# Performance work log

Measured on AMD Instinct MI355X. Metric: run time of the kernel, lower is better.

Reference implementation:

```python
import jax, jax.numpy as jnp
import numpy as np

M_MARGIN = 0.25
GAMMA = 64.0
EPS = 1e-5


def _circle_loss_one_way(enc, dec):
    # enc, dec: [N, D]. Faithful to the torch rotate-concat construction:
    # cos_sim[j, k] = cosine(enc[j], dec[(j + k) % N]); column 0 is the positive.
    N = enc.shape[0]
    dot = enc @ dec.T                                   # [N, N]
    en = jnp.sqrt(jnp.sum(enc * enc, axis=1, keepdims=True))   # [N, 1]
    dn = jnp.sqrt(jnp.sum(dec * dec, axis=1, keepdims=True))   # [N, 1]
    S = dot / (en * dn.T + EPS)                         # [N, N] cosine sims
    r = jnp.arange(N)
    idx = (r[:, None] + r[None, :]) % N                 # [N, N] rolled column index
    cos_sim = jnp.take_along_axis(S, idx, axis=1)       # [N, N]
    sp = cos_sim[:, 0:1]                                # [N, 1] positives (diag of S)
    sn = cos_sim[:, 1:]                                 # [N, N-1] negatives
    ap = jnp.maximum(-jax.lax.stop_gradient(sp) + 1.0 + M_MARGIN, 0.0)
    an = jnp.maximum(jax.lax.stop_gradient(sn) + M_MARGIN, 0.0)
    delta_p = 1.0 - M_MARGIN
    delta_n = M_MARGIN
    logit_p = -ap * (sp - delta_p) * GAMMA              # [N, 1]
    logit_n = an * (sn - delta_n) * GAMMA               # [N, N-1]
    lse_n = jax.nn.logsumexp(logit_n, axis=0)           # [N-1]
    lse_p = jax.nn.logsumexp(logit_p, axis=0)           # [1] (cols of repeated sp are identical)
    return jax.nn.softplus(lse_n + lse_p)               # [N-1]


def reference(encoder_output, decoder_output):
    loss_a = _circle_loss_one_way(encoder_output, decoder_output)
    loss_b = _circle_loss_one_way(decoder_output, encoder_output)
    return jnp.mean((loss_a + loss_b) / 2.0)


def setup_inputs() -> dict:
    key = jax.random.key(0)
    k1, k2 = jax.random.split(key)
    N, D = 8192, 128
    return {
        "encoder_output": jax.random.normal(k1, (N, D), dtype=jnp.float32),
        "decoder_output": jax.random.normal(k2, (N, D), dtype=jnp.float32),
    }
```

## Files before the change

### kernel.cpp

```cpp
#include <hip/hip_runtime.h>
#include <hip/hip_bf16.h>

#define NN 8192

using f32x4 = __attribute__((ext_vector_type(4))) float;

#if __has_builtin(__builtin_amdgcn_exp2f)
#define EXP2(x) __builtin_amdgcn_exp2f(x)
#else
#define EXP2(x) __expf((x) * 0.69314718056f)
#endif

__device__ __forceinline__ void gl_lds16(const void* g, void* l) {
  __builtin_amdgcn_global_load_lds(
      (const __attribute__((address_space(1))) unsigned int*)(unsigned long long)g,
      (__attribute__((address_space(3))) unsigned int*)(unsigned int)(unsigned long long)l,
      16, 0, 0);
}

#define BAR_VMCNT4() asm volatile("s_waitcnt vmcnt(4)\n\ts_barrier" ::: "memory")

#if __has_builtin(__builtin_amdgcn_cvt_pk_fp8_f32)
__device__ __forceinline__ unsigned pk4_fp8(float x0, float x1, float x2, float x3) {
  unsigned w = (unsigned)__builtin_amdgcn_cvt_pk_fp8_f32(x0, x1, 0, false);
  w = (unsigned)__builtin_amdgcn_cvt_pk_fp8_f32(x2, x3, (int)w, true);
  return w;
}
#else
__device__ __forceinline__ unsigned f8_1(float f) {
  unsigned u = __float_as_uint(f);
  unsigned s = (u >> 24) & 0x80u;
  float a = fabsf(f);
  if (a < 0.015625f) {
    unsigned m = (unsigned)rintf(a * 512.0f);
    return s | (m > 7u ? 8u : m);
  }
  if (a > 448.0f) return s | 0x7Eu;
  unsigned au = u & 0x7FFFFFFFu;
  unsigned e = (au >> 23) - 127u + 7u;
  unsigned m23 = au & 0x7FFFFFu;
  unsigned m = m23 >> 20;
  unsigned rem = m23 & 0xFFFFFu;
  if (rem > 0x80000u || (rem == 0x80000u && (m & 1u))) {
    if (++m == 8u) { m = 0u; ++e; }
  }
  return s | (e << 3) | m;
}
__device__ __forceinline__ unsigned pk4_fp8(float x0, float x1, float x2, float x3) {
  return f8_1(x0) | (f8_1(x1) << 8) | (f8_1(x2) << 16) | (f8_1(x3) << 24);
}
#endif

__global__ __launch_bounds__(256) void k_prep(const float* __restrict__ enc,
                                              const float* __restrict__ dec,
                                              uint2* __restrict__ A8,
                                              uint2* __restrict__ B8,
                                              float* __restrict__ logit_p,
                                              float* __restrict__ bandsum,
                                              unsigned* __restrict__ counter) {
  const int t = threadIdx.x;
  const int l16 = t & 15;
  const int row = blockIdx.x * 16 + (t >> 4);
  const int tid = blockIdx.x * 256 + t;
  if (tid < 64 * 256) bandsum[tid] = 0.0f;
  if (tid == 64 * 256) *counter = 0u;

  const float4* e4 = reinterpret_cast<const float4*>(enc) + (size_t)row * 32 + l16 * 2;
  const float4* d4 = reinterpret_cast<const float4*>(dec) + (size_t)row * 32 + l16 * 2;
  float4 e0 = e4[0], e1 = e4[1];
  float4 d0 = d4[0], d1 = d4[1];

  float se = e0.x*e0.x + e0.y*e0.y + e0.z*e0.z + e0.w*e0.w
           + e1.x*e1.x + e1.y*e1.y + e1.z*e1.z + e1.w*e1.w;
  float sd = d0.x*d0.x + d0.y*d0.y + d0.z*d0.z + d0.w*d0.w
           + d1.x*d1.x + d1.y*d1.y + d1.z*d1.z + d1.w*d1.w;
  float sp = e0.x*d0.x + e0.y*d0.y + e0.z*d0.z + e0.w*d0.w
           + e1.x*d1.x + e1.y*d1.y + e1.z*d1.z + e1.w*d1.w;
#pragma unroll
  for (int off = 1; off < 16; off <<= 1) {
    se += __shfl_xor(se, off);
    sd += __shfl_xor(sd, off);
    sp += __shfl_xor(sp, off);
  }
  float ie = rsqrtf(se), id = rsqrtf(sd);

  uint2 ua, ub;
  ua.x = pk4_fp8(e0.x * ie, e0.y * ie, e0.z * ie, e0.w * ie);
  ua.y = pk4_fp8(e1.x * ie, e1.y * ie, e1.z * ie, e1.w * ie);
  ub.x = pk4_fp8(d0.x * id, d0.y * id, d0.z * id, d0.w * id);
  ub.y = pk4_fp8(d1.x * id, d1.y * id, d1.z * id, d1.w * id);
  A8[(size_t)row * 16 + l16] = ua;
  B8[(size_t)row * 16 + l16] = ub;

  if (l16 == 0) {
    float en = se * ie, dn = sd * id;
    float s  = sp / (en * dn + 1e-5f);
    logit_p[row] = -fmaxf(1.25f - s, 0.0f) * (s - 0.75f) * 64.0f;
  }
}

__global__ __launch_bounds__(256, 3) void k_main(const unsigned char* __restrict__ A,
                                                 const unsigned char* __restrict__ B,
                                                 float* __restrict__ bandsum,
                                                 const float* __restrict__ logit_p,
                                                 unsigned* __restrict__ counter,
                                                 float* __restrict__ out) {
  __shared__ __align__(16) unsigned char As[3 * 8192];
  __shared__ __align__(16) unsigned char Bs[3 * 8192];
  __shared__ float part[4][256];
  __shared__ unsigned lastFlag;

  const int t  = threadIdx.x;
  const int T  = blockIdx.x;
  const int sp = blockIdx.y;

#pragma unroll
  for (int q = 0; q < 4; ++q) part[q][t] = 0.0f;

  const int lane = t & 63;
  const int w = t >> 6, wrow = w >> 1, wcol = w & 1;
  const int l15 = lane & 15, quad = lane >> 4;
  const int x3 = l15 & 3;
  const int qh = quad >> 1, ql8 = (quad & 1) * 8;

  const int lg    = (t >> 2) * 128 + (((t & 3) ^ ((t >> 2) & 3)) * 16);
  const int lloff = t * 16;

  const char* Ab = (const char*)A;
  const char* Bb = (const char*)B;

  float dreg[28];
#pragma unroll
  for (int i = 0; i < 28; ++i) dreg[i] = 0.0f;

  const int arow = (wrow * 64 + l15) * 64;
  const int brow = (wcol * 64 + l15) * 64;

  const int s16 = sp * 16;
  const int by0 = s16 / 3;
  const int by1 = (s16 + 16) / 3;
  const int H   = (by1 - by0) * 2;

  {
    const int bx = (by0 + T) & 63;
    const char* Ag = Ab + (size_t)by0 * 16384 + lg;
    const char* Bg = Bb + (size_t)bx * 16384 + lg;
#pragma unroll
    for (int j = 0; j < 2; ++j) {
      gl_lds16(Ag + j * 8192, (char*)As + j * 4096 + lloff);
      gl_lds16(Bg + j * 8192, (char*)Bs + j * 4096 + lloff);
    }
#pragma unroll
    for (int j = 0; j < 2; ++j) {
      gl_lds16(Ag + 64 + j * 8192, (char*)As + 8192 + j * 4096 + lloff);
      gl_lds16(Bg + 64 + j * 8192, (char*)Bs + 8192 + j * 4096 + lloff);
    }
  }
  BAR_VMCNT4();

  f32x4 acc[4][4];
  int cur = 0;

  for (int h = 0; h < H; ++h) {
    if (h + 2 < H) {
      const int hn = h + 2;
      const int by = by0 + (hn >> 1);
      const int bx = (by + T) & 63;
      int r2 = cur + 2; if (r2 >= 3) r2 -= 3;
      const char* Ag = Ab + (size_t)by * 16384 + (hn & 1) * 64 + lg;
      const char* Bg = Bb + (size_t)bx * 16384 + (hn & 1) * 64 + lg;
      char* Ad = (char*)As + r2 * 8192 + lloff;
      char* Bd = (char*)Bs + r2 * 8192 + lloff;
#pragma unroll
      for (int j = 0; j < 2; ++j) {
        gl_lds16(Ag + j * 8192, Ad + j * 4096);
        gl_lds16(Bg + j * 8192, Bd + j * 4096);
      }
    }

    if ((h & 1) == 0) {
      const f32x4 zv = {0.f, 0.f, 0.f, 0.f};
#pragma unroll
      for (int r = 0; r < 4; ++r)
#pragma unroll
        for (int c = 0; c < 4; ++c) acc[r][c] = zv;
    }

    const char* Abuf = (const char*)As + cur * 8192;
    const char* Bbuf = (const char*)Bs + cur * 8192;

#pragma unroll
    for (int ks = 0; ks < 2; ++ks) {
      long a[4], b[4];
      const int off = (((ks * 2 + qh) ^ x3) * 16) + ql8;
#pragma unroll
      for (int r = 0; r < 4; ++r)
        a[r] = *reinterpret_cast<const long*>(Abuf + arow + r * 1024 + off);
#pragma unroll
      for (int c = 0; c < 4; ++c)
        b[c] = *reinterpret_cast<const long*>(Bbuf + brow + c * 1024 + off);
#pragma unroll
      for (int r = 0; r < 4; ++r)
#pragma unroll
        for (int c = 0; c < 4; ++c)
          acc[r][c] = __builtin_amdgcn_mfma_f32_16x16x32_fp8_fp8(a[r], b[c], acc[r][c], 0, 0, 0);
    }

    if (h & 1) {
#pragma unroll
      for (int dlt = -3; dlt <= 3; ++dlt) {
#pragma unroll
        for (int g = 0; g < 4; ++g) {
          float s = 0.0f;
#pragma unroll
          for (int r = 0; r < 4; ++r) {
            int c = r + dlt;
            if (c < 0 || c > 3) continue;
            float sn = acc[r][c][g];
            float an = fmaxf(sn + 0.25f, 0.0f);
            float u  = fmaf(sn, 92.332483f, -23.083121f);
            s += EXP2(an * u);
          }
          dreg[(dlt + 3) * 4 + g] += s;
        }
      }
    }

    BAR_VMCNT4();
    if (++cur == 3) cur = 0;
  }

  const int  Qoff = (wcol - wrow) * 64 + 127;
  const int  v    = l15 - quad * 4;
  const bool leader = (quad == 0) || (l15 <= 3);
  const bool ok1 = (l15 <= 11) && (quad <= 2);
  const bool ok2 = (l15 <= 7)  && (quad <= 1);

#pragma unroll
  for (int dlt = -3; dlt <= 3; ++dlt) {
#pragma unroll
    for (int g = 0; g < 4; ++g) {
      float s = dreg[(dlt + 3) * 4 + g];
      float t1 = __shfl_down(s, 20); s += ok1 ? t1 : 0.0f;
      float t2 = __shfl_down(s, 40); s += ok2 ? t2 : 0.0f;
      int ld = Qoff + dlt * 16 - g + v;
      if (leader) unsafeAtomicAdd(&part[w][ld], s);
    }
  }
  __syncthreads();

  if (t < 255) {
    float vv = part[0][t] + part[1][t] + part[2][t] + part[3][t];
    unsafeAtomicAdd(&bandsum[T * 256 + t], vv);
  }

  __syncthreads();
  if (t == 0) lastFlag = (atomicAdd(counter, 1u) == 767u) ? 1u : 0u;
  __syncthreads();
  if (!lastFlag) return;

  __threadfence();
  float* sm = part[0];

  float lp[32];
#pragma unroll
  for (int k = 0; k < 32; ++k) lp[k] = logit_p[t + 256 * k];

  float m = lp[0];
#pragma unroll
  for (int k = 1; k < 32; ++k) m = fmaxf(m, lp[k]);
#pragma unroll
  for (int off = 32; off; off >>= 1) m = fmaxf(m, __shfl_down(m, off));
  if (lane == 0) sm[w] = m;
  __syncthreads();
  m = fmaxf(fmaxf(sm[0], sm[1]), fmaxf(sm[2], sm[3]));
  __syncthreads();

  float s = 0.0f;
#pragma unroll
  for (int k = 0; k < 32; ++k) s += __expf(lp[k] - m);
#pragma unroll
  for (int off = 32; off; off >>= 1) s += __shfl_down(s, off);
  if (lane == 0) sm[w] = s;
  __syncthreads();
  s = sm[0] + sm[1] + sm[2] + sm[3];
  float lse_p = m + __logf(s);
  __syncthreads();

  const int o  = t & 127;
  const int hi = t >> 7;
  float bs1[32], bs2[32];
#pragma unroll
  for (int k = 0; k < 32; ++k) {
    int Ta = hi + 2 * k;
    bs1[k] = bandsum[Ta * 256 + o + 127];
    bs2[k] = o ? bandsum[((Ta + 1) & 63) * 256 + o - 1] : 0.0f;
  }
  float tacc = 0.0f;
#pragma unroll
  for (int k = 0; k < 32; ++k) {
    if (t == 0 && k == 0) continue;
    float se = bs1[k] + bs2[k];
    float x = __logf(se) + lse_p;
    tacc += fmaxf(x, 0.0f) + __logf(1.0f + __expf(-fabsf(x)));
  }
#pragma unroll
  for (int off = 32; off; off >>= 1) tacc += __shfl_down(tacc, off);
  if (lane == 0) sm[w] = tacc;
  __syncthreads();
  if (t == 0) out[0] = (sm[0] + sm[1] + sm[2] + sm[3]) * (1.0f / 8191.0f);
}

extern "C" void kernel_launch(void* const* d_in, const int* in_sizes, int n_in,
                              void* d_out, int out_size, void* d_ws, size_t ws_size,
                              hipStream_t stream) {
  const float* enc = (const float*)d_in[0];
  const float* dec = (const float*)d_in[1];
  float* ws = (float*)d_ws;

  float*    logit_p = ws;
  float*    bandsum = ws + 8192;
  unsigned* counter = (unsigned*)(ws + 8192 + 16384);
  uint2*    A8      = (uint2*)(ws + 8192 + 16384 + 256);
  uint2*    B8      = (uint2*)((char*)A8 + 1048576);
  float*    out     = (float*)d_out;

  k_prep<<<NN / 16, 256, 0, stream>>>(enc, dec, A8, B8, logit_p, bandsum, counter);
  dim3 grid(64, 12);
  k_main<<<grid, 256, 0, stream>>>((const unsigned char*)A8, (const unsigned char*)B8,
                                   bandsum, logit_p, counter, out);
}
```

Measured before the change: 105.4 us.

## Load MFMA operands directly from global memory instead of LDS triple buffer

Removes the triple-buffered LDS staging, which used global_load_lds copies with barriers. Each wave now reads its fp8 A/B fragments straight from global memory (L1/L2) and processes a whole 128-deep K tile per iteration. This drops LDS traffic, barriers and LDS allocation, which may allow higher occupancy. In exchange every element is loaded redundantly by several waves from cache, and there is no explicit prefetch to overlap load latency with MFMA.

```diff
diff --git a/kernel.cpp b/kernel.cpp
--- a/kernel.cpp
+++ b/kernel.cpp
@@ -10,15 +10,6 @@
 #else
 #define EXP2(x) __expf((x) * 0.69314718056f)
 #endif
-
-__device__ __forceinline__ void gl_lds16(const void* g, void* l) {
-  __builtin_amdgcn_global_load_lds(
-      (const __attribute__((address_space(1))) unsigned int*)(unsigned long long)g,
-      (__attribute__((address_space(3))) unsigned int*)(unsigned int)(unsigned long long)l,
-      16, 0, 0);
-}
-
-#define BAR_VMCNT4() asm volatile("s_waitcnt vmcnt(4)\n\ts_barrier" ::: "memory")
 
 #if __has_builtin(__builtin_amdgcn_cvt_pk_fp8_f32)
 __device__ __forceinline__ unsigned pk4_fp8(float x0, float x1, float x2, float x3) {
@@ -105,8 +96,6 @@
                                                  const float* __restrict__ logit_p,
                                                  unsigned* __restrict__ counter,
                                                  float* __restrict__ out) {
-  __shared__ __align__(16) unsigned char As[3 * 8192];
-  __shared__ __align__(16) unsigned char Bs[3 * 8192];
   __shared__ float part[4][256];
   __shared__ unsigned lastFlag;
 
@@ -120,65 +109,30 @@
   const int lane = t & 63;
   const int w = t >> 6, wrow = w >> 1, wcol = w & 1;
   const int l15 = lane & 15, quad = lane >> 4;
-  const int x3 = l15 & 3;
-  const int qh = quad >> 1, ql8 = (quad & 1) * 8;
-
-  const int lg    = (t >> 2) * 128 + (((t & 3) ^ ((t >> 2) & 3)) * 16);
-  const int lloff = t * 16;
-
+
+  float dreg[28];
+#pragma unroll
+  for (int i = 0; i < 28; ++i) dreg[i] = 0.0f;
+
+  __syncthreads();
+
+  const int aoff = (wrow * 64 + l15) * 128 + quad * 8;
+  const int boff = (wcol * 64 + l15) * 128 + quad * 8;
   const char* Ab = (const char*)A;
   const char* Bb = (const char*)B;
-
-  float dreg[28];
-#pragma unroll
-  for (int i = 0; i < 28; ++i) dreg[i] = 0.0f;
-
-  const int arow = (wrow * 64 + l15) * 64;
-  const int brow = (wcol * 64 + l15) * 64;
 
   const int s16 = sp * 16;
   const int by0 = s16 / 3;
   const int by1 = (s16 + 16) / 3;
-  const int H   = (by1 - by0) * 2;
-
-  {
-    const int bx = (by0 + T) & 63;
-    const char* Ag = Ab + (size_t)by0 * 16384 + lg;
-    const char* Bg = Bb + (size_t)bx * 16384 + lg;
-#pragma unroll
-    for (int j = 0; j < 2; ++j) {
-      gl_lds16(Ag + j * 8192, (char*)As + j * 4096 + lloff);
-      gl_lds16(Bg + j * 8192, (char*)Bs + j * 4096 + lloff);
-    }
-#pragma unroll
-    for (int j = 0; j < 2; ++j) {
-      gl_lds16(Ag + 64 + j * 8192, (char*)As + 8192 + j * 4096 + lloff);
-      gl_lds16(Bg + 64 + j * 8192, (char*)Bs + 8192 + j * 4096 + lloff);
-    }
-  }
-  BAR_VMCNT4();
 
   f32x4 acc[4][4];
-  int cur = 0;
-
-  for (int h = 0; h < H; ++h) {
-    if (h + 2 < H) {
-      const int hn = h + 2;
-      const int by = by0 + (hn >> 1);
-      const int bx = (by + T) & 63;
-      int r2 = cur + 2; if (r2 >= 3) r2 -= 3;
-      const char* Ag = Ab + (size_t)by * 16384 + (hn & 1) * 64 + lg;
-      const char* Bg = Bb + (size_t)bx * 16384 + (hn & 1) * 64 + lg;
-      char* Ad = (char*)As + r2 * 8192 + lloff;
-      char* Bd = (char*)Bs + r2 * 8192 + lloff;
-#pragma unroll
-      for (int j = 0; j < 2; ++j) {
-        gl_lds16(Ag + j * 8192, Ad + j * 4096);
-        gl_lds16(Bg + j * 8192, Bd + j * 4096);
-      }
-    }
-
-    if ((h & 1) == 0) {
+
+  for (int by = by0; by < by1; ++by) {
+    const int bx = (by + T) & 63;
+    const char* Ag = Ab + (size_t)by * 16384 + aoff;
+    const char* Bg = Bb + (size_t)bx * 16384 + boff;
+
+    {
       const f32x4 zv = {0.f, 0.f, 0.f, 0.f};
 #pragma unroll
       for (int r = 0; r < 4; ++r)
@@ -186,19 +140,16 @@
         for (int c = 0; c < 4; ++c) acc[r][c] = zv;
     }
 
-    const char* Abuf = (const char*)As + cur * 8192;
-    const char* Bbuf = (const char*)Bs + cur * 8192;
-
-#pragma unroll
-    for (int ks = 0; ks < 2; ++ks) {
+#pragma unroll
+    for (int ks = 0; ks < 4; ++ks) {
       long a[4], b[4];
-      const int off = (((ks * 2 + qh) ^ x3) * 16) + ql8;
+      const int o = ks * 32;
 #pragma unroll
       for (int r = 0; r < 4; ++r)
-        a[r] = *reinterpret_cast<const long*>(Abuf + arow + r * 1024 + off);
+        a[r] = *reinterpret_cast<const long*>(Ag + r * 2048 + o);
 #pragma unroll
       for (int c = 0; c < 4; ++c)
-        b[c] = *reinterpret_cast<const long*>(Bbuf + brow + c * 1024 + off);
+        b[c] = *reinterpret_cast<const long*>(Bg + c * 2048 + o);
 #pragma unroll
       for (int r = 0; r < 4; ++r)
 #pragma unroll
@@ -206,28 +157,23 @@
           acc[r][c] = __builtin_amdgcn_mfma_f32_16x16x32_fp8_fp8(a[r], b[c], acc[r][c], 0, 0, 0);
     }
 
-    if (h & 1) {
-#pragma unroll
-      for (int dlt = -3; dlt <= 3; ++dlt) {
-#pragma unroll
-        for (int g = 0; g < 4; ++g) {
-          float s = 0.0f;
-#pragma unroll
-          for (int r = 0; r < 4; ++r) {
-            int c = r + dlt;
-            if (c < 0 || c > 3) continue;
-            float sn = acc[r][c][g];
-            float an = fmaxf(sn + 0.25f, 0.0f);
-            float u  = fmaf(sn, 92.332483f, -23.083121f);
-            s += EXP2(an * u);
-          }
-          dreg[(dlt + 3) * 4 + g] += s;
+#pragma unroll
+    for (int dlt = -3; dlt <= 3; ++dlt) {
+#pragma unroll
+      for (int g = 0; g < 4; ++g) {
+        float s = 0.0f;
+#pragma unroll
+        for (int r = 0; r < 4; ++r) {
+          int c = r + dlt;
+          if (c < 0 || c > 3) continue;
+          float sn = acc[r][c][g];
+          float an = fmaxf(sn + 0.25f, 0.0f);
+          float u  = fmaf(sn, 92.332483f, -23.083121f);
+          s += EXP2(an * u);
         }
+        dreg[(dlt + 3) * 4 + g] += s;
       }
     }
-
-    BAR_VMCNT4();
-    if (++cur == 3) cur = 0;
   }
 
   const int  Qoff = (wcol - wrow) * 64 + 127;
```

After: 129.4 us. 1.23x slower.
